# Optimization experiments

Hardware: AMD Instinct MI355X
Metric: run time of the kernel (lower is better)

Reference implementation:

```python
import jax, jax.numpy as jnp
import numpy as np

HEAD_DIM = 128
N_HEADS = 32
N_KV = 8
EPS = 1e-6


def setup_inputs() -> dict:
    key = jax.random.key(0)
    ks = jax.random.split(key, 8)
    B, S, H = 1, 2048, 2560
    hidden_states = jax.random.normal(ks[0], (B, S, H), dtype=jnp.float32)
    # rotary embeddings (any values work for a math reference)
    pos = jnp.arange(S, dtype=jnp.float32)[:, None]
    inv_freq = 1.0 / (10000.0 ** (jnp.arange(0, HEAD_DIM, 2, dtype=jnp.float32) / HEAD_DIM))
    ang = pos * inv_freq[None, :]            # [S, HEAD_DIM/2]
    emb = jnp.concatenate([ang, ang], axis=-1)  # [S, HEAD_DIM]
    cos = jnp.cos(emb)[None]                 # [1, S, HEAD_DIM]
    sin = jnp.sin(emb)[None]
    sc = 0.02
    Wq = jax.random.normal(ks[1], (N_HEADS * HEAD_DIM, H), dtype=jnp.float32) * sc
    Wk = jax.random.normal(ks[2], (N_KV * HEAD_DIM, H), dtype=jnp.float32) * sc
    Wv = jax.random.normal(ks[3], (N_KV * HEAD_DIM, H), dtype=jnp.float32) * sc
    Wo = jax.random.normal(ks[4], (H, N_HEADS * HEAD_DIM), dtype=jnp.float32) * sc
    q_norm_w = jnp.ones((HEAD_DIM,), dtype=jnp.float32)
    k_norm_w = jnp.ones((HEAD_DIM,), dtype=jnp.float32)
    return dict(hidden_states=hidden_states, cos=cos, sin=sin,
                Wq=Wq, Wk=Wk, Wv=Wv, Wo=Wo,
                q_norm_w=q_norm_w, k_norm_w=k_norm_w)


def _rms_norm(x, w):
    var = jnp.mean(x * x, axis=-1, keepdims=True)
    return x * jax.lax.rsqrt(var + EPS) * w


def _rotate_half(x):
    x1, x2 = jnp.split(x, 2, axis=-1)
    return jnp.concatenate([-x2, x1], axis=-1)


def reference(hidden_states, cos, sin, Wq, Wk, Wv, Wo, q_norm_w, k_norm_w):
    B, S, H = hidden_states.shape
    scale = HEAD_DIM ** -0.5
    # projections -> [B, heads, S, D]
    q = (hidden_states @ Wq.T).reshape(B, S, N_HEADS, HEAD_DIM)
    k = (hidden_states @ Wk.T).reshape(B, S, N_KV, HEAD_DIM)
    v = (hidden_states @ Wv.T).reshape(B, S, N_KV, HEAD_DIM)
    q = _rms_norm(q, q_norm_w).transpose(0, 2, 1, 3)   # [B, 32, S, D]
    k = _rms_norm(k, k_norm_w).transpose(0, 2, 1, 3)   # [B, 8, S, D]
    v = v.transpose(0, 2, 1, 3)
    # RoPE (cos/sin broadcast over heads via [:, None])
    c = cos[:, None]
    s = sin[:, None]
    q = q * c + _rotate_half(q) * s
    k = k * c + _rotate_half(k) * s
    # GQA: expand kv heads (repeat_kv)
    rep = N_HEADS // N_KV
    k = jnp.repeat(k, rep, axis=1)  # [B, 32, S, D]
    v = jnp.repeat(v, rep, axis=1)
    # causal SDPA (prefill => is_causal=True, full-length cache)
    scores = jnp.einsum('bhqd,bhkd->bhqk', q, k) * scale
    causal = jnp.tril(jnp.ones((S, S), dtype=bool))
    scores = jnp.where(causal, scores, jnp.finfo(scores.dtype).min)
    probs = jax.nn.softmax(scores, axis=-1)
    out = jnp.einsum('bhqk,bhkd->bhqd', probs, v)      # [B, 32, S, D]
    out = out.transpose(0, 2, 1, 3).reshape(B, S, N_HEADS * HEAD_DIM)
    return out @ Wo.T
```

## Files before the change

kernel.cpp:

```cpp
#include <hip/hip_runtime.h>
#include <hip/hip_bf16.h>

#define S_LEN   2048
#define HID     2560
#define NH      32
#define NKV     8
#define HD      128
#define QDIM    (NH*HD)
#define KVDIM   (NKV*HD)

typedef __attribute__((ext_vector_type(8))) short short8;
typedef __attribute__((ext_vector_type(4))) float f32x4;

__device__ __forceinline__ unsigned short f2bf(float f) {
    unsigned u = __float_as_uint(f);
    u += 0x7fffu + ((u >> 16) & 1u);
    return (unsigned short)(u >> 16);
}
__device__ __forceinline__ float bf2f(unsigned short s) {
    return __uint_as_float(((unsigned)s) << 16);
}
__device__ __forceinline__ unsigned pk2bf(float a, float b) {
    __hip_bfloat162 h = __float22bfloat162_rn(make_float2(a, b));
    union { __hip_bfloat162 h; unsigned u; } c; c.h = h; return c.u;
}
__device__ __forceinline__ void gload16(const void* g, void* l) {
    __builtin_amdgcn_global_load_lds(
        (const __attribute__((address_space(1))) unsigned int*)g,
        (__attribute__((address_space(3))) unsigned int*)l, 16, 0, 0);
}

#define N4_HS  (S_LEN*HID/4)
#define N4_WQ  (QDIM*HID/4)
#define N4_WKV (KVDIM*HID/4)
__global__ __launch_bounds__(256) void cvt4(
    const float* __restrict__ hs, const float* __restrict__ Wq,
    const float* __restrict__ Wk, const float* __restrict__ Wv,
    unsigned short* __restrict__ hsB, unsigned short* __restrict__ WqB,
    unsigned short* __restrict__ WkB, unsigned short* __restrict__ WvB)
{
    int i = blockIdx.x * 256 + threadIdx.x;
    const float* s; unsigned short* d;
    if (i < N4_HS)                          { s = hs; d = hsB; }
    else if (i < N4_HS + N4_WQ)             { i -= N4_HS; s = Wq; d = WqB; }
    else if (i < N4_HS + N4_WQ + N4_WKV)    { i -= N4_HS + N4_WQ; s = Wk; d = WkB; }
    else                                    { i -= N4_HS + N4_WQ + N4_WKV; s = Wv; d = WvB; }
    float4 v = ((const float4*)s)[i];
    uint2 o;
    o.x = pk2bf(v.x, v.y); o.y = pk2bf(v.z, v.w);
    ((uint2*)d)[i] = o;
}

__global__ __launch_bounds__(256) void cvt_f32_bf16(
    const float* __restrict__ s, unsigned short* __restrict__ d, int n4)
{
    int i = blockIdx.x * 256 + threadIdx.x;
    if (i >= n4) return;
    float4 v = ((const float4*)s)[i];
    uint2 o;
    o.x = pk2bf(v.x, v.y); o.y = pk2bf(v.z, v.w);
    ((uint2*)d)[i] = o;
}

struct GemmRegs {
    f32x4 acc[4][4];
};
__device__ __forceinline__ void gemm_core(
    const unsigned short* A, const unsigned short* B, int Kd,
    unsigned short* As, unsigned short* Bs, GemmRegs& R,
    int rowA0, int rowB0, int tid)
{
    const int lane = tid & 63;
    const int l15 = lane & 15, l4 = lane >> 4;
    const int w = tid >> 6;
    const int wr = (w >> 1) * 64, wc = (w & 1) * 64;
    const int sw = l15 & 7;

#pragma unroll
    for (int i = 0; i < 4; i++)
#pragma unroll
        for (int j = 0; j < 4; j++)
            R.acc[i][j] = (f32x4){0.f, 0.f, 0.f, 0.f};

    for (int k0 = 0; k0 < Kd; k0 += 64) {
        __syncthreads();
#pragma unroll
        for (int i = 0; i < 4; i++) {
            int tc = tid + i * 256;
            int r = tc >> 3, cl = tc & 7;
            int cg = cl ^ (r & 7);
            gload16(A + (size_t)(rowA0 + r) * Kd + k0 + cg * 8, &As[tc * 8]);
            gload16(B + (size_t)(rowB0 + r) * Kd + k0 + cg * 8, &Bs[tc * 8]);
        }
        __syncthreads();

#pragma unroll
        for (int ks = 0; ks < 2; ks++) {
            const int kc = (ks * 4 + l4) ^ sw;
            short8 af[4], bf[4];
#pragma unroll
            for (int i = 0; i < 4; i++)
                af[i] = *(const short8*)&As[(wr + i*16 + l15)*64 + kc*8];
#pragma unroll
            for (int j = 0; j < 4; j++)
                bf[j] = *(const short8*)&Bs[(wc + j*16 + l15)*64 + kc*8];
#pragma unroll
            for (int i = 0; i < 4; i++)
#pragma unroll
                for (int j = 0; j < 4; j++)
                    R.acc[i][j] = __builtin_amdgcn_mfma_f32_16x16x32_bf16(
                        af[i], bf[j], R.acc[i][j], 0, 0, 0);
        }
    }
}

__global__ __launch_bounds__(256) void gemm_qkv(
    const unsigned short* __restrict__ A,
    const unsigned short* __restrict__ Wq, const unsigned short* __restrict__ Wk,
    const unsigned short* __restrict__ Wv,
    unsigned short* __restrict__ Qo, unsigned short* __restrict__ Ko,
    unsigned short* __restrict__ VTo)
{
    __shared__ unsigned short As[128*64];
    __shared__ unsigned short Bs[128*64];
    const int bx = blockIdx.x;
    const unsigned short* B;
    if (bx < 32)      B = Wq + (size_t)bx*128*HID;
    else if (bx < 40) B = Wk + (size_t)(bx-32)*128*HID;
    else              B = Wv + (size_t)(bx-40)*128*HID;

    const int tid = threadIdx.x;
    const int lane = tid & 63, w = tid >> 6;
    const int l15 = lane & 15, l4 = lane >> 4;
    const int wr = (w >> 1) * 64, wc = (w & 1) * 64;
    GemmRegs R;
    gemm_core(A, B, HID, As, Bs, R, blockIdx.y * 128, 0, tid);

    if (bx < 40) {
        unsigned short* C; int ldc, cb;
        if (bx < 32) { C = Qo; ldc = QDIM;  cb = bx*128; }
        else         { C = Ko; ldc = KVDIM; cb = (bx-32)*128; }
#pragma unroll
        for (int i = 0; i < 4; i++)
#pragma unroll
            for (int j = 0; j < 4; j++) {
                int row0 = blockIdx.y*128 + wr + i*16 + l4*4;
                int col  = cb + wc + j*16 + l15;
#pragma unroll
                for (int r = 0; r < 4; r++)
                    C[(size_t)(row0 + r) * ldc + col] = f2bf(R.acc[i][j][r]);
            }
    } else {
        const int cbase = (bx - 40) * 128;
#pragma unroll
        for (int i = 0; i < 4; i++)
#pragma unroll
            for (int j = 0; j < 4; j++) {
                int col  = cbase + wc + j*16 + l15;
                int row0 = blockIdx.y*128 + wr + i*16 + l4*4;
                int kvhh = col >> 7, d = col & 127;
                unsigned short* p = VTo + (size_t)kvhh*HD*S_LEN + (size_t)d*S_LEN + row0;
                uint2 pk;
                pk.x = pk2bf(R.acc[i][j][0], R.acc[i][j][1]);
                pk.y = pk2bf(R.acc[i][j][2], R.acc[i][j][3]);
                *(uint2*)p = pk;
            }
    }
}

__global__ __launch_bounds__(256) void gemm_out(
    const unsigned short* __restrict__ A, const unsigned short* __restrict__ B,
    float* __restrict__ C, int N, int Kd)
{
    __shared__ unsigned short As[64*64];
    __shared__ unsigned short Bs[128*64];
    const int tid = threadIdx.x;
    const int lane = tid & 63, w = tid >> 6;
    const int l15 = lane & 15, l4 = lane >> 4;
    const int wr = (w >> 1) * 32, wc = (w & 1) * 64;
    const int rowA0 = blockIdx.y * 64, rowB0 = blockIdx.x * 128;
    const int sw = l15 & 7;

    f32x4 acc[2][4];
#pragma unroll
    for (int i = 0; i < 2; i++)
#pragma unroll
        for (int j = 0; j < 4; j++) acc[i][j] = (f32x4){0.f, 0.f, 0.f, 0.f};

    for (int k0 = 0; k0 < Kd; k0 += 64) {
        __syncthreads();
#pragma unroll
        for (int i = 0; i < 2; i++) {
            int tc = tid + i * 256;
            int r = tc >> 3, cl = tc & 7;
            int cg = cl ^ (r & 7);
            gload16(A + (size_t)(rowA0 + r) * Kd + k0 + cg * 8, &As[tc * 8]);
        }
#pragma unroll
        for (int i = 0; i < 4; i++) {
            int tc = tid + i * 256;
            int r = tc >> 3, cl = tc & 7;
            int cg = cl ^ (r & 7);
            gload16(B + (size_t)(rowB0 + r) * Kd + k0 + cg * 8, &Bs[tc * 8]);
        }
        __syncthreads();

#pragma unroll
        for (int ks = 0; ks < 2; ks++) {
            const int kc = (ks * 4 + l4) ^ sw;
            short8 af[2], bf[4];
#pragma unroll
            for (int i = 0; i < 2; i++)
                af[i] = *(const short8*)&As[(wr + i*16 + l15)*64 + kc*8];
#pragma unroll
            for (int j = 0; j < 4; j++)
                bf[j] = *(const short8*)&Bs[(wc + j*16 + l15)*64 + kc*8];
#pragma unroll
            for (int i = 0; i < 2; i++)
#pragma unroll
                for (int j = 0; j < 4; j++)
                    acc[i][j] = __builtin_amdgcn_mfma_f32_16x16x32_bf16(
                        af[i], bf[j], acc[i][j], 0, 0, 0);
        }
    }

#pragma unroll
    for (int i = 0; i < 2; i++)
#pragma unroll
        for (int j = 0; j < 4; j++) {
            int row0 = rowA0 + wr + i*16 + l4*4;
            int col  = rowB0 + wc + j*16 + l15;
#pragma unroll
            for (int r = 0; r < 4; r++)
                C[(size_t)(row0 + r) * N + col] = acc[i][j][r];
        }
}

__global__ __launch_bounds__(256) void rmsnorm_rope_bf16(
    unsigned short* __restrict__ X, const float* __restrict__ w,
    const float* __restrict__ ct, const float* __restrict__ st, int nheads)
{
    int wid  = (blockIdx.x * blockDim.x + threadIdx.x) >> 6;
    int lane = threadIdx.x & 63;
    int s = wid / nheads;
    int h = wid - s * nheads;
    unsigned short* x = X + (size_t)s * (nheads * HD) + h * HD;

    float x1 = bf2f(x[lane]);
    float x2 = bf2f(x[lane + 64]);
    float ss = x1*x1 + x2*x2;
#pragma unroll
    for (int off = 32; off > 0; off >>= 1) ss += __shfl_xor(ss, off, 64);
    float r = rsqrtf(ss * (1.0f/128.0f) + 1e-6f);
    float n1 = x1 * r * w[lane];
    float n2 = x2 * r * w[lane + 64];
    float c1 = ct[s*HD + lane],      s1 = st[s*HD + lane];
    float c2 = ct[s*HD + lane + 64], s2 = st[s*HD + lane + 64];
    x[lane]      = f2bf(n1*c1 - n2*s1);
    x[lane + 64] = f2bf(n2*c2 + n1*s2);
}

__global__ __launch_bounds__(256, 3) void flash_mfma(
    const unsigned short* __restrict__ Q, const unsigned short* __restrict__ K,
    const unsigned short* __restrict__ VT, unsigned short* __restrict__ O)
{
    const int pb = blockIdx.x;
    const int h = blockIdx.y, kvh = h >> 2;
    const int tid = threadIdx.x;
    const int w = tid >> 6, lane = tid & 63;
    const int l15 = lane & 15, l4 = lane >> 4;

    __shared__ unsigned short Ks[64*128];
    __shared__ unsigned short Vt[128*64];
    __shared__ unsigned short Ps[4*16*72];
    __shared__ float Lw[4][16];

    const float scale2 = 0.08838834764831845f * 1.4426950408889634f;
    const float M2 = 17.3f;
    unsigned short* Pw = &Ps[w * 16 * 72];
    const unsigned short* VTh = VT + (size_t)kvh * HD * S_LEN;

#pragma unroll 1
    for (int phase = 0; phase < 2; phase++) {
        const int qt = phase ? pb : (31 - pb);
        const int q0 = qt * 64;

        short8 qa[4];
        {
            const unsigned short* qg = Q + (size_t)(q0 + w*16 + l15) * QDIM + h * HD;
#pragma unroll
            for (int ka = 0; ka < 4; ka++)
                qa[ka] = *(const short8*)(qg + ka*32 + l4*8);
        }

        const f32x4 zero = {0.f, 0.f, 0.f, 0.f};
        f32x4 accO[8];
#pragma unroll
        for (int j = 0; j < 8; j++) accO[j] = zero;
        float lsum = 0.f;

        for (int t = 0; t <= qt; t++) {
            const int c0 = t * 64;
            __syncthreads();
            {
#pragma unroll
                for (int i = 0; i < 4; i++) {
                    int tc = tid + i * 256;
                    int r = tc >> 4, cl = tc & 15;
                    int cg = cl ^ (r & 7);
                    gload16(K + (size_t)(c0 + r) * KVDIM + kvh * HD + cg * 8,
                            &Ks[tc * 8]);
                }
            }
            {
#pragma unroll
                for (int i = 0; i < 4; i++) {
                    int tc = tid + i * 256;
                    int r = tc >> 3, cl = tc & 7;
                    int cg = cl ^ (r & 7);
                    gload16(VTh + (size_t)r * S_LEN + c0 + cg * 8, &Vt[tc * 8]);
                }
            }
            __syncthreads();

            f32x4 sc[4];
#pragma unroll
            for (int mt = 0; mt < 4; mt++) sc[mt] = zero;
#pragma unroll
            for (int ka = 0; ka < 4; ka++) {
#pragma unroll
                for (int mt = 0; mt < 4; mt++) {
                    int row = mt*16 + l15;
                    int cs = (ka*4 + l4) ^ (row & 7);
                    short8 kb = *(const short8*)&Ks[row*128 + cs*8];
                    sc[mt] = __builtin_amdgcn_mfma_f32_16x16x32_bf16(kb, qa[ka], sc[mt], 0, 0, 0);
                }
            }

            const int qglob = q0 + w*16 + l15;
            const bool diag = (t == qt);
#pragma unroll
            for (int mt = 0; mt < 4; mt++) {
                float pv[4];
#pragma unroll
                for (int r = 0; r < 4; r++) {
                    int kvg = c0 + mt*16 + l4*4 + r;
                    float e = __builtin_amdgcn_exp2f(fmaf(sc[mt][r], scale2, -M2));
                    pv[r] = (!diag || kvg <= qglob) ? e : 0.f;
                    lsum += pv[r];
                }
                uint2 pk;
                pk.x = pk2bf(pv[0], pv[1]);
                pk.y = pk2bf(pv[2], pv[3]);
                *(uint2*)&Pw[l15*72 + mt*16 + l4*4] = pk;
            }

#pragma unroll
            for (int ks = 0; ks < 2; ks++) {
                short8 pf = *(const short8*)&Pw[l15*72 + ks*32 + l4*8];
                const int cs = (ks*4 + l4) ^ (l15 & 7);
#pragma unroll
                for (int dt = 0; dt < 8; dt++) {
                    short8 vf = *(const short8*)&Vt[(dt*16 + l15)*64 + cs*8];
                    accO[dt] = __builtin_amdgcn_mfma_f32_16x16x32_bf16(pf, vf, accO[dt], 0, 0, 0);
                }
            }
        }

        lsum += __shfl_xor(lsum, 16, 64);
        lsum += __shfl_xor(lsum, 32, 64);
        if (l4 == 0) Lw[w][l15] = lsum;
        f32x4 linv;
#pragma unroll
        for (int r = 0; r < 4; r++) linv[r] = 1.0f / Lw[w][l4*4 + r];

#pragma unroll
        for (int dt = 0; dt < 8; dt++)
#pragma unroll
            for (int r = 0; r < 4; r++) {
                int row_l = w*16 + l4*4 + r;
                O[(size_t)(q0 + row_l) * QDIM + h*HD + dt*16 + l15] =
                    f2bf(accO[dt][r] * linv[r]);
            }
    }
}

extern "C" void kernel_launch(void* const* d_in, const int* in_sizes, int n_in,
                              void* d_out, int out_size, void* d_ws, size_t ws_size,
                              hipStream_t stream)
{
    const float* hs   = (const float*)d_in[0];
    const float* cosb = (const float*)d_in[1];
    const float* sinb = (const float*)d_in[2];
    const float* Wq   = (const float*)d_in[3];
    const float* Wk   = (const float*)d_in[4];
    const float* Wv   = (const float*)d_in[5];
    const float* Wo   = (const float*)d_in[6];
    const float* qw   = (const float*)d_in[7];
    const float* kw   = (const float*)d_in[8];
    float* out = (float*)d_out;

    char* ws = (char*)d_ws;
    unsigned short* hsB = (unsigned short*)(ws);
    unsigned short* WqB = (unsigned short*)(ws + 10485760);
    unsigned short* WkB = (unsigned short*)(ws + 31457280);
    unsigned short* WvB = (unsigned short*)(ws + 36700160);
    unsigned short* KB  = (unsigned short*)(ws + 41943040);
    unsigned short* VT  = (unsigned short*)(ws + 46137344);
    unsigned short* WoB = (unsigned short*)(ws + 41943040);
    unsigned short* QB  = (unsigned short*)(ws + 62914560);
    unsigned short* CB  = (unsigned short*)(ws + 18874368);

    {
        int n4 = N4_HS + N4_WQ + 2 * N4_WKV;
        cvt4<<<(n4+255)/256, 256, 0, stream>>>(hs, Wq, Wk, Wv, hsB, WqB, WkB, WvB);
    }

    gemm_qkv<<<dim3(48, S_LEN/128), 256, 0, stream>>>(hsB, WqB, WkB, WvB, QB, KB, VT);

    rmsnorm_rope_bf16<<<S_LEN*NH/4,  256, 0, stream>>>(QB, qw, cosb, sinb, NH);
    rmsnorm_rope_bf16<<<S_LEN*NKV/4, 256, 0, stream>>>(KB, kw, cosb, sinb, NKV);

    flash_mfma<<<dim3(16, NH), 256, 0, stream>>>(QB, KB, VT, CB);

    cvt_f32_bf16<<<(HID*QDIM/4+255)/256, 256, 0, stream>>>(Wo, WoB, HID*QDIM/4);

    gemm_out<<<dim3(HID/128, S_LEN/64), 256, 0, stream>>>(CB, WoB, out, HID, QDIM);
}
```

Measured before the change: 373.4 us.

## Rewrite QKV GEMM as 256x256 double-buffered pipelined kernel with block swizzle

Replaces the 128x128 single-buffered QKV projection GEMM with a 256x256 tile, 512-thread kernel. It double-buffers LDS and interleaves global-to-LDS staging of the next K-slices with MFMA phases, using manual s_barrier/s_waitcnt and setprio. It also remaps block indices so neighbouring blocks share A/B tiles in cache. The aim is to hide global load latency and raise arithmetic intensity. The cost is 128KB of LDS per block and a 192-block grid, which may underfill the GPU's CUs.

```diff
diff --git a/kernel.cpp b/kernel.cpp
--- a/kernel.cpp
+++ b/kernel.cpp
@@ -62,107 +62,146 @@
     ((uint2*)d)[i] = o;
 }
 
-struct GemmRegs {
-    f32x4 acc[4][4];
-};
-__device__ __forceinline__ void gemm_core(
-    const unsigned short* A, const unsigned short* B, int Kd,
-    unsigned short* As, unsigned short* Bs, GemmRegs& R,
-    int rowA0, int rowB0, int tid)
-{
-    const int lane = tid & 63;
-    const int l15 = lane & 15, l4 = lane >> 4;
-    const int w = tid >> 6;
-    const int wr = (w >> 1) * 64, wc = (w & 1) * 64;
-    const int sw = l15 & 7;
-
-#pragma unroll
-    for (int i = 0; i < 4; i++)
-#pragma unroll
-        for (int j = 0; j < 4; j++)
-            R.acc[i][j] = (f32x4){0.f, 0.f, 0.f, 0.f};
-
-    for (int k0 = 0; k0 < Kd; k0 += 64) {
-        __syncthreads();
-#pragma unroll
-        for (int i = 0; i < 4; i++) {
-            int tc = tid + i * 256;
-            int r = tc >> 3, cl = tc & 7;
-            int cg = cl ^ (r & 7);
-            gload16(A + (size_t)(rowA0 + r) * Kd + k0 + cg * 8, &As[tc * 8]);
-            gload16(B + (size_t)(rowB0 + r) * Kd + k0 + cg * 8, &Bs[tc * 8]);
-        }
-        __syncthreads();
-
-#pragma unroll
-        for (int ks = 0; ks < 2; ks++) {
-            const int kc = (ks * 4 + l4) ^ sw;
-            short8 af[4], bf[4];
-#pragma unroll
-            for (int i = 0; i < 4; i++)
-                af[i] = *(const short8*)&As[(wr + i*16 + l15)*64 + kc*8];
-#pragma unroll
-            for (int j = 0; j < 4; j++)
-                bf[j] = *(const short8*)&Bs[(wc + j*16 + l15)*64 + kc*8];
-#pragma unroll
-            for (int i = 0; i < 4; i++)
-#pragma unroll
-                for (int j = 0; j < 4; j++)
-                    R.acc[i][j] = __builtin_amdgcn_mfma_f32_16x16x32_bf16(
-                        af[i], bf[j], R.acc[i][j], 0, 0, 0);
-        }
-    }
-}
-
-__global__ __launch_bounds__(256) void gemm_qkv(
+#define STG_A(b, h, t) do {                                                  \
+    _Pragma("unroll")                                                        \
+    for (int c_ = 0; c_ < 2; c_++) {                                         \
+        int r_ = c_*128 + (h)*64 + (tid >> 3);                               \
+        int cg_ = (tid & 7) ^ (r_ & 7);                                      \
+        gload16(Ag + (size_t)(rowA0 + r_) * HID + (size_t)(t)*64 + cg_*8,    \
+                &As[b][r_*64 + (tid & 7)*8]);                                \
+    } } while (0)
+
+#define STG_B(b, h, t) do {                                                  \
+    _Pragma("unroll")                                                        \
+    for (int c_ = 0; c_ < 2; c_++) {                                         \
+        int r_ = c_*128 + ((tid >> 8) << 6) + (h)*32 + ((tid >> 3) & 31);    \
+        int cg_ = (tid & 7) ^ (r_ & 7);                                      \
+        gload16(Bg + (size_t)(rowB0 + r_) * HID + (size_t)(t)*64 + cg_*8,    \
+                &Bs[b][r_*64 + (tid & 7)*8]);                                \
+    } } while (0)
+
+#define PHASE(b, rh, ch, STAGE_STMT, WV) do {                                \
+    short8 af_[4][2], bf_[2][2];                                             \
+    _Pragma("unroll")                                                        \
+    for (int i_ = 0; i_ < 4; i_++) {                                         \
+        int row_ = wr + (rh)*64 + i_*16 + l15;                               \
+        _Pragma("unroll")                                                    \
+        for (int kk_ = 0; kk_ < 2; kk_++)                                    \
+            af_[i_][kk_] = *(const short8*)                                  \
+                &As[b][row_*64 + (((kk_*4 + l4) ^ sw8))*8];                  \
+    }                                                                        \
+    _Pragma("unroll")                                                        \
+    for (int j_ = 0; j_ < 2; j_++) {                                         \
+        int row_ = wc + (ch)*32 + j_*16 + l15;                               \
+        _Pragma("unroll")                                                    \
+        for (int kk_ = 0; kk_ < 2; kk_++)                                    \
+            bf_[j_][kk_] = *(const short8*)                                  \
+                &Bs[b][row_*64 + (((kk_*4 + l4) ^ sw8))*8];                  \
+    }                                                                        \
+    STAGE_STMT;                                                              \
+    asm volatile("s_barrier" ::: "memory");                                  \
+    asm volatile("s_waitcnt lgkmcnt(0)" ::: "memory");                       \
+    __builtin_amdgcn_s_setprio(1);                                           \
+    _Pragma("unroll")                                                        \
+    for (int kk_ = 0; kk_ < 2; kk_++)                                        \
+        _Pragma("unroll")                                                    \
+        for (int i_ = 0; i_ < 4; i_++)                                       \
+            _Pragma("unroll")                                                \
+            for (int j_ = 0; j_ < 2; j_++)                                   \
+                acc[(rh)*4 + i_][(ch)*2 + j_] =                              \
+                    __builtin_amdgcn_mfma_f32_16x16x32_bf16(                 \
+                        af_[i_][kk_], bf_[j_][kk_],                          \
+                        acc[(rh)*4 + i_][(ch)*2 + j_], 0, 0, 0);             \
+    __builtin_amdgcn_s_setprio(0);                                           \
+    if ((WV) == 1) {                                                         \
+        if (p2v) asm volatile("s_waitcnt vmcnt(4)" ::: "memory");            \
+        else     asm volatile("s_waitcnt vmcnt(0)" ::: "memory");            \
+    } else if ((WV) == 2) {                                                  \
+        asm volatile("s_waitcnt vmcnt(4)" ::: "memory");                     \
+    }                                                                        \
+    asm volatile("s_barrier" ::: "memory");                                  \
+} while (0)
+
+__global__ __launch_bounds__(512, 2) void gemm_qkv(
     const unsigned short* __restrict__ A,
     const unsigned short* __restrict__ Wq, const unsigned short* __restrict__ Wk,
     const unsigned short* __restrict__ Wv,
     unsigned short* __restrict__ Qo, unsigned short* __restrict__ Ko,
     unsigned short* __restrict__ VTo)
 {
-    __shared__ unsigned short As[128*64];
-    __shared__ unsigned short Bs[128*64];
-    const int bx = blockIdx.x;
-    const unsigned short* B;
-    if (bx < 32)      B = Wq + (size_t)bx*128*HID;
-    else if (bx < 40) B = Wk + (size_t)(bx-32)*128*HID;
-    else              B = Wv + (size_t)(bx-40)*128*HID;
+    __shared__ unsigned short As[2][256*64];
+    __shared__ unsigned short Bs[2][256*64];
+
+    const int flat = blockIdx.y * 24 + blockIdx.x;
+    const int swz  = (flat & 7) * 24 + (flat >> 3);
+    const int bx = swz % 24, by = swz / 24;
+
+    const unsigned short* Bg; int rowB0;
+    if (bx < 16)      { Bg = Wq; rowB0 = bx * 256; }
+    else if (bx < 20) { Bg = Wk; rowB0 = (bx-16) * 256; }
+    else              { Bg = Wv; rowB0 = (bx-20) * 256; }
+    const unsigned short* Ag = A;
+    const int rowA0 = by * 256;
 
     const int tid = threadIdx.x;
     const int lane = tid & 63, w = tid >> 6;
     const int l15 = lane & 15, l4 = lane >> 4;
-    const int wr = (w >> 1) * 64, wc = (w & 1) * 64;
-    GemmRegs R;
-    gemm_core(A, B, HID, As, Bs, R, blockIdx.y * 128, 0, tid);
-
-    if (bx < 40) {
+    const int wr = (w >> 2) * 128;
+    const int wc = (w & 3) * 64;
+    const int sw8 = l15 & 7;
+
+    f32x4 acc[8][4];
+#pragma unroll
+    for (int i = 0; i < 8; i++)
+#pragma unroll
+        for (int j = 0; j < 4; j++) acc[i][j] = (f32x4){0.f, 0.f, 0.f, 0.f};
+
+    STG_A(0,0,0); STG_B(0,0,0); STG_A(0,1,0); STG_B(0,1,0);
+    STG_A(1,0,1); STG_B(1,0,1);
+    asm volatile("s_waitcnt vmcnt(4)" ::: "memory");
+    asm volatile("s_barrier" ::: "memory");
+
+#pragma unroll 1
+    for (int t = 0; t < HID/64; t += 2) {
+        const bool p2v = (t + 2 < HID/64);
+        const bool p3v = (t + 3 < HID/64);
+        PHASE(0, 0, 0, { STG_A(1,1,t+1); STG_B(1,1,t+1); }, 0);
+        PHASE(0, 0, 1, {}, 0);
+        PHASE(0, 1, 0, { if (p2v) STG_A(0,0,t+2); }, 0);
+        PHASE(0, 1, 1, { if (p2v) STG_B(0,0,t+2); }, 1);
+        PHASE(1, 0, 0, { if (p2v) { STG_A(0,1,t+2); STG_B(0,1,t+2); } }, 0);
+        PHASE(1, 0, 1, {}, 0);
+        PHASE(1, 1, 0, { if (p3v) STG_A(1,0,t+3); }, 0);
+        PHASE(1, 1, 1, { if (p3v) STG_B(1,0,t+3); }, 2);
+    }
+
+    if (bx < 20) {
         unsigned short* C; int ldc, cb;
-        if (bx < 32) { C = Qo; ldc = QDIM;  cb = bx*128; }
-        else         { C = Ko; ldc = KVDIM; cb = (bx-32)*128; }
-#pragma unroll
-        for (int i = 0; i < 4; i++)
+        if (bx < 16) { C = Qo; ldc = QDIM;  cb = bx*256; }
+        else         { C = Ko; ldc = KVDIM; cb = (bx-16)*256; }
+#pragma unroll
+        for (int i = 0; i < 8; i++)
 #pragma unroll
             for (int j = 0; j < 4; j++) {
-                int row0 = blockIdx.y*128 + wr + i*16 + l4*4;
+                int row0 = by*256 + wr + i*16 + l4*4;
                 int col  = cb + wc + j*16 + l15;
 #pragma unroll
                 for (int r = 0; r < 4; r++)
-                    C[(size_t)(row0 + r) * ldc + col] = f2bf(R.acc[i][j][r]);
+                    C[(size_t)(row0 + r) * ldc + col] = f2bf(acc[i][j][r]);
             }
     } else {
-        const int cbase = (bx - 40) * 128;
-#pragma unroll
-        for (int i = 0; i < 4; i++)
+        const int cbase = (bx - 20) * 256;
+#pragma unroll
+        for (int i = 0; i < 8; i++)
 #pragma unroll
             for (int j = 0; j < 4; j++) {
                 int col  = cbase + wc + j*16 + l15;
-                int row0 = blockIdx.y*128 + wr + i*16 + l4*4;
+                int row0 = by*256 + wr + i*16 + l4*4;
                 int kvhh = col >> 7, d = col & 127;
                 unsigned short* p = VTo + (size_t)kvhh*HD*S_LEN + (size_t)d*S_LEN + row0;
                 uint2 pk;
-                pk.x = pk2bf(R.acc[i][j][0], R.acc[i][j][1]);
-                pk.y = pk2bf(R.acc[i][j][2], R.acc[i][j][3]);
+                pk.x = pk2bf(acc[i][j][0], acc[i][j][1]);
+                pk.y = pk2bf(acc[i][j][2], acc[i][j][3]);
                 *(uint2*)p = pk;
             }
     }
@@ -416,7 +455,7 @@
         cvt4<<<(n4+255)/256, 256, 0, stream>>>(hs, Wq, Wk, Wv, hsB, WqB, WkB, WvB);
     }
 
-    gemm_qkv<<<dim3(48, S_LEN/128), 256, 0, stream>>>(hsB, WqB, WkB, WvB, QB, KB, VT);
+    gemm_qkv<<<dim3(24, S_LEN/256), 512, 0, stream>>>(hsB, WqB, WkB, WvB, QB, KB, VT);
 
     rmsnorm_rope_bf16<<<S_LEN*NH/4,  256, 0, stream>>>(QB, qw, cosb, sinb, NH);
     rmsnorm_rope_bf16<<<S_LEN*NKV/4, 256, 0, stream>>>(KB, kw, cosb, sinb, NKV);
```

After: 402.7 us. +7.8%, slower.

## Double-buffer LDS tiles in the output GEMM and flash attention loops

Applied to the files above, without the earlier changes.

Both the output-projection GEMM and the flash attention kernel now keep two LDS buffers for their K-loop tiles. The next tile's global-to-LDS load is issued right after the barrier, before the MFMA work on the current tile, so the two can overlap and one barrier per iteration is dropped. The cost is doubled LDS for K/V and A/B tiles. Because of that, the flash kernel's launch-bounds occupancy hint drops from 3 to 2 blocks, which may reduce latency hiding across workgroups.

```diff
diff --git a/kernel.cpp b/kernel.cpp
--- a/kernel.cpp
+++ b/kernel.cpp
@@ -168,12 +168,31 @@
     }
 }
 
+#define OSTG(it_, b_) do {                                                   \
+    int k0_ = (it_) * 64;                                                    \
+    _Pragma("unroll")                                                        \
+    for (int i_ = 0; i_ < 2; i_++) {                      \
+        int tc_ = tid + i_ * 256;                                            \
+        int r_ = tc_ >> 3, cl_ = tc_ & 7;                                    \
+        int cg_ = cl_ ^ (r_ & 7);                                            \
+        gload16(A + (size_t)(rowA0 + r_) * Kd + k0_ + cg_ * 8,               \
+                &As[b_][tc_ * 8]);                                           \
+    }                                                                        \
+    _Pragma("unroll")                                                        \
+    for (int i_ = 0; i_ < 4; i_++) {                     \
+        int tc_ = tid + i_ * 256;                                            \
+        int r_ = tc_ >> 3, cl_ = tc_ & 7;                                    \
+        int cg_ = cl_ ^ (r_ & 7);                                            \
+        gload16(B + (size_t)(rowB0 + r_) * Kd + k0_ + cg_ * 8,               \
+                &Bs[b_][tc_ * 8]);                                           \
+    } } while (0)
+
 __global__ __launch_bounds__(256) void gemm_out(
     const unsigned short* __restrict__ A, const unsigned short* __restrict__ B,
     float* __restrict__ C, int N, int Kd)
 {
-    __shared__ unsigned short As[64*64];
-    __shared__ unsigned short Bs[128*64];
+    __shared__ unsigned short As[2][64*64];
+    __shared__ unsigned short Bs[2][128*64];
     const int tid = threadIdx.x;
     const int lane = tid & 63, w = tid >> 6;
     const int l15 = lane & 15, l4 = lane >> 4;
@@ -187,23 +206,13 @@
 #pragma unroll
         for (int j = 0; j < 4; j++) acc[i][j] = (f32x4){0.f, 0.f, 0.f, 0.f};
 
-    for (int k0 = 0; k0 < Kd; k0 += 64) {
+    const int nk = Kd / 64;
+    OSTG(0, 0);
+
+    for (int it = 0; it < nk; it++) {
+        const int cur = it & 1;
         __syncthreads();
-#pragma unroll
-        for (int i = 0; i < 2; i++) {
-            int tc = tid + i * 256;
-            int r = tc >> 3, cl = tc & 7;
-            int cg = cl ^ (r & 7);
-            gload16(A + (size_t)(rowA0 + r) * Kd + k0 + cg * 8, &As[tc * 8]);
-        }
-#pragma unroll
-        for (int i = 0; i < 4; i++) {
-            int tc = tid + i * 256;
-            int r = tc >> 3, cl = tc & 7;
-            int cg = cl ^ (r & 7);
-            gload16(B + (size_t)(rowB0 + r) * Kd + k0 + cg * 8, &Bs[tc * 8]);
-        }
-        __syncthreads();
+        if (it + 1 < nk) OSTG(it + 1, cur ^ 1);
 
 #pragma unroll
         for (int ks = 0; ks < 2; ks++) {
@@ -211,10 +220,10 @@
             short8 af[2], bf[4];
 #pragma unroll
             for (int i = 0; i < 2; i++)
-                af[i] = *(const short8*)&As[(wr + i*16 + l15)*64 + kc*8];
+                af[i] = *(const short8*)&As[cur][(wr + i*16 + l15)*64 + kc*8];
 #pragma unroll
             for (int j = 0; j < 4; j++)
-                bf[j] = *(const short8*)&Bs[(wc + j*16 + l15)*64 + kc*8];
+                bf[j] = *(const short8*)&Bs[cur][(wc + j*16 + l15)*64 + kc*8];
 #pragma unroll
             for (int i = 0; i < 2; i++)
 #pragma unroll
@@ -260,7 +269,29 @@
     x[lane + 64] = f2bf(n2*c2 + n1*s2);
 }
 
-__global__ __launch_bounds__(256, 3) void flash_mfma(
+#define FSTG_K(t_, b_) do {                                                  \
+    int c0_ = (t_) * 64;                                                     \
+    _Pragma("unroll")                                                        \
+    for (int i_ = 0; i_ < 4; i_++) {                                         \
+        int tc_ = tid + i_ * 256;                                            \
+        int r_ = tc_ >> 4, cl_ = tc_ & 15;                                   \
+        int cg_ = cl_ ^ (r_ & 7);                                            \
+        gload16(K + (size_t)(c0_ + r_) * KVDIM + kvh * HD + cg_ * 8,         \
+                &Ks[b_][tc_ * 8]);                                           \
+    } } while (0)
+
+#define FSTG_V(t_, b_) do {                                                  \
+    int c0_ = (t_) * 64;                                                     \
+    _Pragma("unroll")                                                        \
+    for (int i_ = 0; i_ < 4; i_++) {                                         \
+        int tc_ = tid + i_ * 256;                                            \
+        int r_ = tc_ >> 3, cl_ = tc_ & 7;                                    \
+        int cg_ = cl_ ^ (r_ & 7);                                            \
+        gload16(VTh + (size_t)r_ * S_LEN + c0_ + cg_ * 8,                    \
+                &Vt[b_][tc_ * 8]);                                           \
+    } } while (0)
+
+__global__ __launch_bounds__(256, 2) void flash_mfma(
     const unsigned short* __restrict__ Q, const unsigned short* __restrict__ K,
     const unsigned short* __restrict__ VT, unsigned short* __restrict__ O)
 {
@@ -270,8 +301,8 @@
     const int w = tid >> 6, lane = tid & 63;
     const int l15 = lane & 15, l4 = lane >> 4;
 
-    __shared__ unsigned short Ks[64*128];
-    __shared__ unsigned short Vt[128*64];
+    __shared__ unsigned short Ks[2][64*128];
+    __shared__ unsigned short Vt[2][128*64];
     __shared__ unsigned short Ps[4*16*72];
     __shared__ float Lw[4][16];
 
@@ -293,6 +324,9 @@
                 qa[ka] = *(const short8*)(qg + ka*32 + l4*8);
         }
 
+        __syncthreads();
+        FSTG_K(0, 0); FSTG_V(0, 0);
+
         const f32x4 zero = {0.f, 0.f, 0.f, 0.f};
         f32x4 accO[8];
 #pragma unroll
@@ -301,27 +335,9 @@
 
         for (int t = 0; t <= qt; t++) {
             const int c0 = t * 64;
+            const int cur = t & 1;
             __syncthreads();
-            {
-#pragma unroll
-                for (int i = 0; i < 4; i++) {
-                    int tc = tid + i * 256;
-                    int r = tc >> 4, cl = tc & 15;
-                    int cg = cl ^ (r & 7);
-                    gload16(K + (size_t)(c0 + r) * KVDIM + kvh * HD + cg * 8,
-                            &Ks[tc * 8]);
-                }
-            }
-            {
-#pragma unroll
-                for (int i = 0; i < 4; i++) {
-                    int tc = tid + i * 256;
-                    int r = tc >> 3, cl = tc & 7;
-                    int cg = cl ^ (r & 7);
-                    gload16(VTh + (size_t)r * S_LEN + c0 + cg * 8, &Vt[tc * 8]);
-                }
-            }
-            __syncthreads();
+            if (t < qt) { FSTG_K(t + 1, cur ^ 1); FSTG_V(t + 1, cur ^ 1); }
 
             f32x4 sc[4];
 #pragma unroll
@@ -332,7 +348,7 @@
                 for (int mt = 0; mt < 4; mt++) {
                     int row = mt*16 + l15;
                     int cs = (ka*4 + l4) ^ (row & 7);
-                    short8 kb = *(const short8*)&Ks[row*128 + cs*8];
+                    short8 kb = *(const short8*)&Ks[cur][row*128 + cs*8];
                     sc[mt] = __builtin_amdgcn_mfma_f32_16x16x32_bf16(kb, qa[ka], sc[mt], 0, 0, 0);
                 }
             }
@@ -361,7 +377,7 @@
                 const int cs = (ks*4 + l4) ^ (l15 & 7);
 #pragma unroll
                 for (int dt = 0; dt < 8; dt++) {
-                    short8 vf = *(const short8*)&Vt[(dt*16 + l15)*64 + cs*8];
+                    short8 vf = *(const short8*)&Vt[cur][(dt*16 + l15)*64 + cs*8];
                     accO[dt] = __builtin_amdgcn_mfma_f32_16x16x32_bf16(pf, vf, accO[dt], 0, 0, 0);
                 }
             }
```

Measured after the change: 384.1 us. 2.9% more time.

## Fuse Q/K RMSNorm and RoPE into the QKV projection GEMM epilogue

Applied to the files above, without the earlier changes.

Moves the per-head RMSNorm and rotary embedding into the QKV GEMM epilogue. Row sums of squares are reduced across lanes and across the two column warps through shared memory, and the rotate-half partner is exchanged through a swizzled shared buffer. This removes two extra kernel launches and a full read-modify-write pass over Q and K in global memory. The cost is extra syncs and shared-memory traffic in the GEMM epilogue. The rotated partner value is also read back at bf16 precision.

```diff
diff --git a/kernel.cpp b/kernel.cpp
--- a/kernel.cpp
+++ b/kernel.cpp
@@ -118,11 +118,16 @@
     const unsigned short* __restrict__ A,
     const unsigned short* __restrict__ Wq, const unsigned short* __restrict__ Wk,
     const unsigned short* __restrict__ Wv,
+    const float* __restrict__ ct, const float* __restrict__ st,
+    const float* __restrict__ qw, const float* __restrict__ kw,
     unsigned short* __restrict__ Qo, unsigned short* __restrict__ Ko,
     unsigned short* __restrict__ VTo)
 {
-    __shared__ unsigned short As[128*64];
-    __shared__ unsigned short Bs[128*64];
+    __shared__ unsigned short Sh[128*128];
+    __shared__ float part[4][4][4][4];
+    unsigned short* As = Sh;
+    unsigned short* Bs = Sh + 128*64;
+
     const int bx = blockIdx.x;
     const unsigned short* B;
     if (bx < 32)      B = Wq + (size_t)bx*128*HID;
@@ -137,19 +142,69 @@
     gemm_core(A, B, HID, As, Bs, R, blockIdx.y * 128, 0, tid);
 
     if (bx < 40) {
+        const float* W = (bx < 32) ? qw : kw;
         unsigned short* C; int ldc, cb;
         if (bx < 32) { C = Qo; ldc = QDIM;  cb = bx*128; }
         else         { C = Ko; ldc = KVDIM; cb = (bx-32)*128; }
+
+        float ssq[4][4];
 #pragma unroll
         for (int i = 0; i < 4; i++)
 #pragma unroll
-            for (int j = 0; j < 4; j++) {
-                int row0 = blockIdx.y*128 + wr + i*16 + l4*4;
-                int col  = cb + wc + j*16 + l15;
+            for (int r = 0; r < 4; r++) {
+                float s = 0.f;
+#pragma unroll
+                for (int j = 0; j < 4; j++)
+                    s += R.acc[i][j][r] * R.acc[i][j][r];
+#pragma unroll
+                for (int off = 1; off < 16; off <<= 1)
+                    s += __shfl_xor(s, off, 64);
+                ssq[i][r] = s;
+            }
+        if (l15 == 0) {
+#pragma unroll
+            for (int i = 0; i < 4; i++)
 #pragma unroll
                 for (int r = 0; r < 4; r++)
-                    C[(size_t)(row0 + r) * ldc + col] = f2bf(R.acc[i][j][r]);
-            }
+                    part[w][i][l4][r] = ssq[i][r];
+        }
+        __syncthreads();
+
+#pragma unroll
+        for (int i = 0; i < 4; i++)
+#pragma unroll
+            for (int r = 0; r < 4; r++) {
+                float rv = rsqrtf((ssq[i][r] + part[w ^ 1][i][l4][r])
+                                  * (1.0f/128.0f) + 1e-6f);
+                int row_l = wr + i*16 + l4*4 + r;
+                int sx = (row_l & 7) << 3;
+#pragma unroll
+                for (int j = 0; j < 4; j++) {
+                    int col = wc + j*16 + l15;
+                    float v = R.acc[i][j][r] * rv * W[col];
+                    R.acc[i][j][r] = v;
+                    Sh[row_l*128 + (col ^ sx)] = f2bf(v);
+                }
+            }
+        __syncthreads();
+
+        const float sgn = (wc == 0) ? -1.0f : 1.0f;
+#pragma unroll
+        for (int i = 0; i < 4; i++)
+#pragma unroll
+            for (int j = 0; j < 4; j++)
+#pragma unroll
+                for (int r = 0; r < 4; r++) {
+                    int row_l = wr + i*16 + l4*4 + r;
+                    int srow  = blockIdx.y*128 + row_l;
+                    int col   = wc + j*16 + l15;
+                    int sx    = (row_l & 7) << 3;
+                    float xo  = bf2f(Sh[row_l*128 + ((col ^ 64) ^ sx)]);
+                    float c   = ct[srow*HD + col];
+                    float sn  = st[srow*HD + col];
+                    float o   = R.acc[i][j][r] * c + sgn * xo * sn;
+                    C[(size_t)srow * ldc + cb + col] = f2bf(o);
+                }
     } else {
         const int cbase = (bx - 40) * 128;
 #pragma unroll
@@ -234,30 +289,6 @@
             for (int r = 0; r < 4; r++)
                 C[(size_t)(row0 + r) * N + col] = acc[i][j][r];
         }
-}
-
-__global__ __launch_bounds__(256) void rmsnorm_rope_bf16(
-    unsigned short* __restrict__ X, const float* __restrict__ w,
-    const float* __restrict__ ct, const float* __restrict__ st, int nheads)
-{
-    int wid  = (blockIdx.x * blockDim.x + threadIdx.x) >> 6;
-    int lane = threadIdx.x & 63;
-    int s = wid / nheads;
-    int h = wid - s * nheads;
-    unsigned short* x = X + (size_t)s * (nheads * HD) + h * HD;
-
-    float x1 = bf2f(x[lane]);
-    float x2 = bf2f(x[lane + 64]);
-    float ss = x1*x1 + x2*x2;
-#pragma unroll
-    for (int off = 32; off > 0; off >>= 1) ss += __shfl_xor(ss, off, 64);
-    float r = rsqrtf(ss * (1.0f/128.0f) + 1e-6f);
-    float n1 = x1 * r * w[lane];
-    float n2 = x2 * r * w[lane + 64];
-    float c1 = ct[s*HD + lane],      s1 = st[s*HD + lane];
-    float c2 = ct[s*HD + lane + 64], s2 = st[s*HD + lane + 64];
-    x[lane]      = f2bf(n1*c1 - n2*s1);
-    x[lane + 64] = f2bf(n2*c2 + n1*s2);
 }
 
 __global__ __launch_bounds__(256, 3) void flash_mfma(
@@ -416,10 +447,8 @@
         cvt4<<<(n4+255)/256, 256, 0, stream>>>(hs, Wq, Wk, Wv, hsB, WqB, WkB, WvB);
     }
 
-    gemm_qkv<<<dim3(48, S_LEN/128), 256, 0, stream>>>(hsB, WqB, WkB, WvB, QB, KB, VT);
-
-    rmsnorm_rope_bf16<<<S_LEN*NH/4,  256, 0, stream>>>(QB, qw, cosb, sinb, NH);
-    rmsnorm_rope_bf16<<<S_LEN*NKV/4, 256, 0, stream>>>(KB, kw, cosb, sinb, NKV);
+    gemm_qkv<<<dim3(48, S_LEN/128), 256, 0, stream>>>(
+        hsB, WqB, WkB, WvB, cosb, sinb, qw, kw, QB, KB, VT);
 
     flash_mfma<<<dim3(16, NH), 256, 0, stream>>>(QB, KB, VT, CB);
 
```

Result: slower. 395.5 us (+5.9%).
